# Kernel optimization log

Hardware: AMD Instinct MI355X
Metric: run time of the kernel (lower is better)

The kernel has to match this reference:

```python
import jax, jax.numpy as jnp
import numpy as np

N = 131072
HIDDEN = 20
N_HID = 7  # layers [3, 20*8, 2] -> 9 Linear layers: in(3,20), 7 hidden(20,20), out(20,2)


def _xavier(k, fan_in, fan_out):
    lim = np.sqrt(6.0 / (fan_in + fan_out)).astype(np.float32)
    return jax.random.uniform(k, (fan_in, fan_out), jnp.float32, -lim, lim)


def setup_inputs() -> dict:
    key = jax.random.key(0)
    ks = jax.random.split(key, 6 + N_HID)
    x = jax.random.normal(ks[0], (N, 1), jnp.float32)
    y = jax.random.normal(ks[1], (N, 1), jnp.float32)
    t = jax.random.normal(ks[2], (N, 1), jnp.float32)
    W_in = _xavier(ks[3], 3, HIDDEN)
    b_in = jnp.zeros((HIDDEN,), jnp.float32)
    W_hid = jnp.stack([_xavier(ks[4 + i], HIDDEN, HIDDEN) for i in range(N_HID)])
    b_hid = jnp.zeros((N_HID, HIDDEN), jnp.float32)
    W_out = _xavier(ks[4 + N_HID], HIDDEN, 2)
    b_out = jnp.zeros((2,), jnp.float32)
    lam1 = jnp.array([1.0], jnp.float32)   # lambda_1 (convective coefficient)
    lam2 = jnp.array([0.01], jnp.float32)  # lambda_2 (viscosity)
    return {"x": x, "y": y, "t": t, "W_in": W_in, "b_in": b_in,
            "W_hid": W_hid, "b_hid": b_hid, "W_out": W_out, "b_out": b_out,
            "lam1": lam1, "lam2": lam2}


def reference(x, y, t, W_in, b_in, W_hid, b_hid, W_out, b_out, lam1, lam2):
    z = jnp.concatenate([x, y, t], axis=1)  # (N, 3)

    def net(zz):  # zz: (3,) -> (2,) = (psi, p)
        h = jnp.tanh(zz @ W_in + b_in)
        for i in range(N_HID):
            h = jnp.tanh(h @ W_hid[i] + b_hid[i])
        return h @ W_out + b_out

    psi_fn = lambda zz: net(zz)[0]
    p_fn = lambda zz: net(zz)[1]
    g_psi = jax.grad(psi_fn)          # (3,): psi_x, psi_y, psi_t
    H_psi = jax.jacfwd(g_psi)         # (3,3): H[a,b] = psi_{ab}
    T_psi = jax.jacfwd(H_psi)         # (3,3,3): T[a,b,c] = psi_{abc}
    g_p = jax.grad(p_fn)              # (3,): p_x, p_y, p_t

    def per_point(zz):
        pv = p_fn(zz)
        gp = g_p(zz)
        g = g_psi(zz)
        H = H_psi(zz)
        T = T_psi(zz)
        # u = psi_y, v = -psi_x (axis 0=x, 1=y, 2=t)
        return jnp.stack([
            g[1], -g[0], pv,                # u, v, p
            H[1, 2], H[1, 0], H[1, 1],      # u_t, u_x, u_y
            T[1, 0, 0], T[1, 1, 1],         # u_xx, u_yy
            -H[0, 2], -H[0, 0], -H[0, 1],   # v_t, v_x, v_y
            -T[0, 0, 0], -T[0, 1, 1],       # v_xx, v_yy
            gp[0], gp[1],                   # p_x, p_y
        ])

    D = jax.vmap(per_point)(z)  # (N, 15)
    (u, v, p, u_t, u_x, u_y, u_xx, u_yy,
     v_t, v_x, v_y, v_xx, v_yy, p_x, p_y) = [D[:, i:i + 1] for i in range(15)]
    l1 = lam1[0]
    l2 = lam2[0]
    f_u = u_t + l1 * (u * u_x + v * u_y) + p_x - l2 * (u_xx + u_yy)
    f_v = v_t + l1 * (u * v_x + v * v_y) + p_y - l2 * (v_xx + v_yy)
    return (u, v, p, f_u, f_v)
```

## Files before the change

### kernel.cpp

```cpp
#include <hip/hip_runtime.h>

typedef float  f32x4  __attribute__((ext_vector_type(4)));
typedef short  bf16x8 __attribute__((ext_vector_type(8)));
typedef unsigned int u32;
typedef u32 u32x4 __attribute__((ext_vector_type(4)));

#define HID  20
#define NLAY 7
#define NC   11
#define PTS  16

__device__ __forceinline__ float tanh_derivs(float a, float& d1, float& d2, float& d3) {
    const float e = __expf(2.0f * a);
    const float s = 1.0f - __fdividef(2.0f, e + 1.0f);
    d1 = 1.0f - s * s;
    d2 = -2.0f * s * d1;
    d3 = -2.0f * (d1 * d1 + s * d2);
    return s;
}

__device__ __forceinline__ void jet_activate(const float* a, float* nv) {
    float d1, d2, d3;
    const float s = tanh_derivs(a[0], d1, d2, d3);
    const float gx = a[1], gy = a[2], gt = a[3];
    const float hxx = a[4], hxy = a[5], hyy = a[6];
    const float hxt = a[7], hyt = a[8];
    const float g2 = gx * gx + gy * gy;
    nv[0] = s;
    nv[1] = d1 * gx;  nv[2] = d1 * gy;  nv[3] = d1 * gt;
    nv[4] = fmaf(d2, gx * gx, d1 * hxx);
    nv[5] = fmaf(d2, gx * gy, d1 * hxy);
    nv[6] = fmaf(d2, gy * gy, d1 * hyy);
    nv[7] = fmaf(d2, gx * gt, d1 * hxt);
    nv[8] = fmaf(d2, gy * gt, d1 * hyt);
    nv[9]  = d3 * gx * g2 + d2 * (3.f * gx * hxx + 2.f * gy * hxy + gx * hyy) + d1 * a[9];
    nv[10] = d3 * gy * g2 + d2 * (3.f * gy * hyy + 2.f * gx * hxy + gy * hxx) + d1 * a[10];
}

__device__ __forceinline__ void pack_pair(float v0, float v1, u32& wh, u32& wl) {
    const u32 b0 = __float_as_uint(v0);
    const u32 b1 = __float_as_uint(v1);
    wh = (b0 >> 16) | (b1 & 0xFFFF0000u);
    const float l0 = v0 - __uint_as_float(b0 & 0xFFFF0000u);
    const float l1 = v1 - __uint_as_float(b1 & 0xFFFF0000u);
    wl = (__float_as_uint(l0) >> 16) | (__float_as_uint(l1) & 0xFFFF0000u);
}

__device__ __forceinline__ void input_neuron(int j, float xv, float yv, float tv,
                                             const float* __restrict__ W_in,
                                             const float* __restrict__ b_in, float* nv) {
    const float w0 = W_in[j], w1 = W_in[HID + j], w2 = W_in[2 * HID + j];
    const float a0 = fmaf(xv, w0, fmaf(yv, w1, fmaf(tv, w2, b_in[j])));
    float d1, d2, d3;
    const float s = tanh_derivs(a0, d1, d2, d3);
    const float g2w = w0 * w0 + w1 * w1;
    nv[0] = s;        nv[1] = d1 * w0;  nv[2] = d1 * w1;  nv[3] = d1 * w2;
    nv[4] = d2 * w0 * w0; nv[5] = d2 * w0 * w1; nv[6] = d2 * w1 * w1;
    nv[7] = d2 * w0 * w2; nv[8] = d2 * w1 * w2;
    nv[9] = d3 * w0 * g2w; nv[10] = d3 * w1 * g2w;
}

__global__ void wfrag_setup(const float* __restrict__ W_hid,
                            const float* __restrict__ b_hid,
                            unsigned* __restrict__ wsu)
{
    const int l = threadIdx.x;
    const int g = l >> 4, m = l & 15;
    for (int layer = 0; layer < NLAY; ++layer) {
        for (int jt = 0; jt < 2; ++jt) {
            const int j = jt * 16 + m;
            unsigned hi[8], lo[8];
            for (int e = 0; e < 8; ++e) {
                const int k = (e < 4) ? (4 * g + e) : (16 + 4 * g + (e - 4));
                float w = 0.0f;
                if (j < HID) {
                    if (k < HID)       w = W_hid[(layer * HID + k) * HID + j];
                    else if (k == HID) w = b_hid[layer * HID + j];
                }
                const unsigned hb = __float_as_uint(w) & 0xFFFF0000u;
                const float lf = w - __uint_as_float(hb);
                hi[e] = hb >> 16;
                lo[e] = __float_as_uint(lf) >> 16;
            }
            unsigned* ph = wsu + (((layer * 2 + jt) * 2 + 0) * 64 + l) * 4;
            unsigned* pl = wsu + (((layer * 2 + jt) * 2 + 1) * 64 + l) * 4;
            for (int r = 0; r < 4; ++r) {
                ph[r] = hi[2 * r] | (hi[2 * r + 1] << 16);
                pl[r] = lo[2 * r] | (lo[2 * r + 1] << 16);
            }
        }
    }
}

__global__ void __launch_bounds__(64)
pinn_mfma_reg(const float* __restrict__ xs, const float* __restrict__ ys, const float* __restrict__ ts,
              const float* __restrict__ W_in, const float* __restrict__ b_in,
              const float* __restrict__ W_out, const float* __restrict__ b_out,
              const float* __restrict__ lam1p, const float* __restrict__ lam2p,
              const unsigned* __restrict__ wsu,
              float* __restrict__ out, int N)
{
    const int l  = threadIdx.x;
    const int g  = l >> 4, pt = l & 15;
    const int idx0 = blockIdx.x * PTS;
    const int pi = min(idx0 + pt, N - 1);

    u32x4 Bh[NC], Bl[NC];

    const float xv = xs[pi], yv = ys[pi], tv = ts[pi];
    #pragma unroll
    for (int pr = 0; pr < 2; ++pr) {
        float nvA[NC], nvB[NC];
        input_neuron(4 * g + 2 * pr,     xv, yv, tv, W_in, b_in, nvA);
        input_neuron(4 * g + 2 * pr + 1, xv, yv, tv, W_in, b_in, nvB);
        #pragma unroll
        for (int c = 0; c < NC; ++c) {
            u32 th, tl;
            pack_pair(nvA[c], nvB[c], th, tl);
            Bh[c][pr] = th; Bl[c][pr] = tl;
        }
    }
    if (g == 0) {
        #pragma unroll
        for (int pr = 0; pr < 2; ++pr) {
            float nvA[NC], nvB[NC];
            input_neuron(16 + 2 * pr,     xv, yv, tv, W_in, b_in, nvA);
            input_neuron(16 + 2 * pr + 1, xv, yv, tv, W_in, b_in, nvB);
            #pragma unroll
            for (int c = 0; c < NC; ++c) {
                u32 th, tl;
                pack_pair(nvA[c], nvB[c], th, tl);
                Bh[c][2 + pr] = th; Bl[c][2 + pr] = tl;
            }
        }
    } else {
        #pragma unroll
        for (int c = 0; c < NC; ++c) { Bh[c][2] = 0u; Bh[c][3] = 0u; Bl[c][2] = 0u; Bl[c][3] = 0u; }
    }
    Bh[0][2] = (g == 1) ? 0x3F80u : Bh[0][2];
    Bl[0][2] = (g == 1) ? 0u      : Bl[0][2];

    const u32x4* wp = (const u32x4*)wsu;
    u32x4 f0 = wp[((0 * 2 + 0) * 2 + 0) * 64 + l];
    u32x4 f1 = wp[((0 * 2 + 0) * 2 + 1) * 64 + l];
    u32x4 f2 = wp[((0 * 2 + 1) * 2 + 0) * 64 + l];
    u32x4 f3 = wp[((0 * 2 + 1) * 2 + 1) * 64 + l];

    #pragma unroll 1
    for (int layer = 0; layer < NLAY; ++layer) {
        const int nl = (layer + 1 < NLAY) ? layer + 1 : layer;
        u32x4 n0 = wp[((nl * 2 + 0) * 2 + 0) * 64 + l];
        u32x4 n1 = wp[((nl * 2 + 0) * 2 + 1) * 64 + l];
        u32x4 n2 = wp[((nl * 2 + 1) * 2 + 0) * 64 + l];
        u32x4 n3 = wp[((nl * 2 + 1) * 2 + 1) * 64 + l];

        const bf16x8 ah0 = __builtin_bit_cast(bf16x8, f0);
        const bf16x8 al0 = __builtin_bit_cast(bf16x8, f1);
        const bf16x8 ah1 = __builtin_bit_cast(bf16x8, f2);
        const bf16x8 al1 = __builtin_bit_cast(bf16x8, f3);

        f32x4 acc1[NC], acc2[NC];
        #pragma unroll
        for (int c = 0; c < NC; ++c) {
            const bf16x8 bh = __builtin_bit_cast(bf16x8, Bh[c]);
            const bf16x8 bl = __builtin_bit_cast(bf16x8, Bl[c]);
            const f32x4 z = (f32x4){0.f, 0.f, 0.f, 0.f};
            f32x4 a1 = __builtin_amdgcn_mfma_f32_16x16x32_bf16(ah0, bh, z, 0, 0, 0);
            a1 = __builtin_amdgcn_mfma_f32_16x16x32_bf16(ah0, bl, a1, 0, 0, 0);
            a1 = __builtin_amdgcn_mfma_f32_16x16x32_bf16(al0, bh, a1, 0, 0, 0);
            acc1[c] = a1;
            f32x4 a2 = __builtin_amdgcn_mfma_f32_16x16x32_bf16(ah1, bh, z, 0, 0, 0);
            a2 = __builtin_amdgcn_mfma_f32_16x16x32_bf16(ah1, bl, a2, 0, 0, 0);
            a2 = __builtin_amdgcn_mfma_f32_16x16x32_bf16(al1, bh, a2, 0, 0, 0);
            acc2[c] = a2;
        }

        #pragma unroll
        for (int pr = 0; pr < 2; ++pr) {
            float aA[NC], aB[NC], nvA[NC], nvB[NC];
            #pragma unroll
            for (int c = 0; c < NC; ++c) { aA[c] = acc1[c][2 * pr]; aB[c] = acc1[c][2 * pr + 1]; }
            jet_activate(aA, nvA);
            jet_activate(aB, nvB);
            #pragma unroll
            for (int c = 0; c < NC; ++c) {
                u32 th, tl;
                pack_pair(nvA[c], nvB[c], th, tl);
                Bh[c][pr] = th; Bl[c][pr] = tl;
            }
        }
        #pragma unroll
        for (int pr = 0; pr < 2; ++pr) {
            float aA[NC], aB[NC], nvA[NC], nvB[NC];
            #pragma unroll
            for (int c = 0; c < NC; ++c) { aA[c] = acc2[c][2 * pr]; aB[c] = acc2[c][2 * pr + 1]; }
            jet_activate(aA, nvA);
            jet_activate(aB, nvB);
            #pragma unroll
            for (int c = 0; c < NC; ++c) {
                u32 th, tl;
                pack_pair(nvA[c], nvB[c], th, tl);
                Bh[c][2 + pr] = th; Bl[c][2 + pr] = tl;
            }
        }
        Bh[0][2] = (g == 1) ? 0x3F80u : Bh[0][2];
        Bl[0][2] = (g == 1) ? 0u      : Bl[0][2];

        f0 = n0; f1 = n1; f2 = n2; f3 = n3;
    }

    float su = 0, sv = 0, sp = 0, spx = 0, spy = 0, svx = 0;
    float sux = 0, suy = 0, svt = 0, sut = 0, slx = 0, sly = 0;

    #pragma unroll
    for (int q = 0; q < 4; ++q) {
        {
            const int j = 4 * g + q;
            const float w0 = W_out[2 * j], w1 = W_out[2 * j + 1];
            float r[NC];
            #pragma unroll
            for (int c = 0; c < NC; ++c) {
                if (c == 3) { r[c] = 0.0f; continue; }
                const u32 wh = Bh[c][q >> 1], wl = Bl[c][q >> 1];
                const u32 hh = (q & 1) ? (wh & 0xFFFF0000u) : (wh << 16);
                const u32 ll = (q & 1) ? (wl & 0xFFFF0000u) : (wl << 16);
                r[c] = __uint_as_float(hh) + __uint_as_float(ll);
            }
            sp  = fmaf(w1, r[0], sp);
            sv  = fmaf(w0, r[1], sv);    spx = fmaf(w1, r[1], spx);
            su  = fmaf(w0, r[2], su);    spy = fmaf(w1, r[2], spy);
            svx = fmaf(w0, r[4], svx);
            sux = fmaf(w0, r[5], sux);
            suy = fmaf(w0, r[6], suy);
            svt = fmaf(w0, r[7], svt);
            sut = fmaf(w0, r[8], sut);
            slx = fmaf(w0, r[9], slx);
            sly = fmaf(w0, r[10], sly);
        }
        {
            const int j2 = 16 + 4 * g + q;
            const int jc = (j2 < HID) ? j2 : 0;
            const float valid = (j2 < HID) ? 1.0f : 0.0f;
            const float w0 = W_out[2 * jc] * valid, w1 = W_out[2 * jc + 1] * valid;
            float r[NC];
            #pragma unroll
            for (int c = 0; c < NC; ++c) {
                if (c == 3) { r[c] = 0.0f; continue; }
                const u32 wh = Bh[c][2 + (q >> 1)], wl = Bl[c][2 + (q >> 1)];
                const u32 hh = (q & 1) ? (wh & 0xFFFF0000u) : (wh << 16);
                const u32 ll = (q & 1) ? (wl & 0xFFFF0000u) : (wl << 16);
                r[c] = __uint_as_float(hh) + __uint_as_float(ll);
            }
            sp  = fmaf(w1, r[0], sp);
            sv  = fmaf(w0, r[1], sv);    spx = fmaf(w1, r[1], spx);
            su  = fmaf(w0, r[2], su);    spy = fmaf(w1, r[2], spy);
            svx = fmaf(w0, r[4], svx);
            sux = fmaf(w0, r[5], sux);
            suy = fmaf(w0, r[6], suy);
            svt = fmaf(w0, r[7], svt);
            sut = fmaf(w0, r[8], sut);
            slx = fmaf(w0, r[9], slx);
            sly = fmaf(w0, r[10], sly);
        }
    }

    #define RED_(x) x += __shfl_xor(x, 16); x += __shfl_xor(x, 32)
    RED_(su); RED_(sv); RED_(sp); RED_(spx); RED_(spy); RED_(svx);
    RED_(sux); RED_(suy); RED_(svt); RED_(sut); RED_(slx); RED_(sly);
    #undef RED_

    if (g == 0 && idx0 + pt < N) {
        const float l1 = lam1p[0], l2 = lam2p[0];
        const float u = su, v = -sv, p = sp + b_out[1];
        const float fu = sut + l1 * (u * sux + v * suy) + spx - l2 * sly;
        const float fv = -svt + l1 * (u * (-svx) + v * (-sux)) + spy + l2 * slx;
        out[idx0 + pt]         = u;
        out[N + idx0 + pt]     = v;
        out[2 * N + idx0 + pt] = p;
        out[3 * N + idx0 + pt] = fu;
        out[4 * N + idx0 + pt] = fv;
    }
}

extern "C" void kernel_launch(void* const* d_in, const int* in_sizes, int n_in,
                              void* d_out, int out_size, void* d_ws, size_t ws_size,
                              hipStream_t stream) {
    const float* xs    = (const float*)d_in[0];
    const float* ys    = (const float*)d_in[1];
    const float* ts    = (const float*)d_in[2];
    const float* W_in  = (const float*)d_in[3];
    const float* b_in  = (const float*)d_in[4];
    const float* W_hid = (const float*)d_in[5];
    const float* b_hid = (const float*)d_in[6];
    const float* W_out = (const float*)d_in[7];
    const float* b_out = (const float*)d_in[8];
    const float* lam1  = (const float*)d_in[9];
    const float* lam2  = (const float*)d_in[10];
    float* out = (float*)d_out;

    const int N = in_sizes[0];
    wfrag_setup<<<1, 64, 0, stream>>>(W_hid, b_hid, (unsigned*)d_ws);
    const int grid = (N + PTS - 1) / PTS;
    pinn_mfma_reg<<<grid, 64, 0, stream>>>(xs, ys, ts, W_in, b_in, W_out, b_out,
                                           lam1, lam2, (const unsigned*)d_ws, out, N);
}
```

Before: 136.4 us.

## Drop low-bf16 split for third-derivative channels and peel final layer

Packing now uses the hardware v_cvt_pk_bf16_f32 instruction instead of manual bit masking. The two third-derivative channels (9,10) are kept only as a single bf16 high part, which removes their low-part MFMAs and packing work in every layer. The last hidden layer is peeled out of the loop and its activations are fed straight into the output projection in fp32, skipping the final pack and unpack. The risk is reduced precision in the third-derivative terms, which feed the viscosity part of the residual.

```diff
diff --git a/kernel.cpp b/kernel.cpp
--- a/kernel.cpp
+++ b/kernel.cpp
@@ -37,13 +37,17 @@
     nv[10] = d3 * gy * g2 + d2 * (3.f * gy * hyy + 2.f * gx * hxy + gy * hxx) + d1 * a[10];
 }
 
+__device__ __forceinline__ u32 cvt_pk_bf16(float a, float b) {
+    u32 r;
+    asm("v_cvt_pk_bf16_f32 %0, %1, %2" : "=v"(r) : "v"(a), "v"(b));
+    return r;
+}
+
 __device__ __forceinline__ void pack_pair(float v0, float v1, u32& wh, u32& wl) {
-    const u32 b0 = __float_as_uint(v0);
-    const u32 b1 = __float_as_uint(v1);
-    wh = (b0 >> 16) | (b1 & 0xFFFF0000u);
-    const float l0 = v0 - __uint_as_float(b0 & 0xFFFF0000u);
-    const float l1 = v1 - __uint_as_float(b1 & 0xFFFF0000u);
-    wl = (__float_as_uint(l0) >> 16) | (__float_as_uint(l1) & 0xFFFF0000u);
+    wh = cvt_pk_bf16(v0, v1);
+    const float h0 = __uint_as_float(wh << 16);
+    const float h1 = __uint_as_float(wh & 0xFFFF0000u);
+    wl = cvt_pk_bf16(v0 - h0, v1 - h1);
 }
 
 __device__ __forceinline__ void input_neuron(int j, float xv, float yv, float tv,
@@ -115,9 +119,13 @@
         input_neuron(4 * g + 2 * pr + 1, xv, yv, tv, W_in, b_in, nvB);
         #pragma unroll
         for (int c = 0; c < NC; ++c) {
-            u32 th, tl;
-            pack_pair(nvA[c], nvB[c], th, tl);
-            Bh[c][pr] = th; Bl[c][pr] = tl;
+            if (c < 9) {
+                u32 th, tl;
+                pack_pair(nvA[c], nvB[c], th, tl);
+                Bh[c][pr] = th; Bl[c][pr] = tl;
+            } else {
+                Bh[c][pr] = cvt_pk_bf16(nvA[c], nvB[c]);
+            }
         }
     }
     if (g == 0) {
@@ -128,9 +136,13 @@
             input_neuron(16 + 2 * pr + 1, xv, yv, tv, W_in, b_in, nvB);
             #pragma unroll
             for (int c = 0; c < NC; ++c) {
-                u32 th, tl;
-                pack_pair(nvA[c], nvB[c], th, tl);
-                Bh[c][2 + pr] = th; Bl[c][2 + pr] = tl;
+                if (c < 9) {
+                    u32 th, tl;
+                    pack_pair(nvA[c], nvB[c], th, tl);
+                    Bh[c][2 + pr] = th; Bl[c][2 + pr] = tl;
+                } else {
+                    Bh[c][2 + pr] = cvt_pk_bf16(nvA[c], nvB[c]);
+                }
             }
         }
     } else {
@@ -141,18 +153,18 @@
     Bl[0][2] = (g == 1) ? 0u      : Bl[0][2];
 
     const u32x4* wp = (const u32x4*)wsu;
-    u32x4 f0 = wp[((0 * 2 + 0) * 2 + 0) * 64 + l];
-    u32x4 f1 = wp[((0 * 2 + 0) * 2 + 1) * 64 + l];
-    u32x4 f2 = wp[((0 * 2 + 1) * 2 + 0) * 64 + l];
-    u32x4 f3 = wp[((0 * 2 + 1) * 2 + 1) * 64 + l];
+    u32x4 f0 = wp[0 * 64 + l];
+    u32x4 f1 = wp[1 * 64 + l];
+    u32x4 f2 = wp[2 * 64 + l];
+    u32x4 f3 = wp[3 * 64 + l];
 
     #pragma unroll 1
-    for (int layer = 0; layer < NLAY; ++layer) {
-        const int nl = (layer + 1 < NLAY) ? layer + 1 : layer;
-        u32x4 n0 = wp[((nl * 2 + 0) * 2 + 0) * 64 + l];
-        u32x4 n1 = wp[((nl * 2 + 0) * 2 + 1) * 64 + l];
-        u32x4 n2 = wp[((nl * 2 + 1) * 2 + 0) * 64 + l];
-        u32x4 n3 = wp[((nl * 2 + 1) * 2 + 1) * 64 + l];
+    for (int layer = 0; layer < NLAY - 1; ++layer) {
+        const int nl = layer + 1;
+        u32x4 n0 = wp[(nl * 4 + 0) * 64 + l];
+        u32x4 n1 = wp[(nl * 4 + 1) * 64 + l];
+        u32x4 n2 = wp[(nl * 4 + 2) * 64 + l];
+        u32x4 n3 = wp[(nl * 4 + 3) * 64 + l];
 
         const bf16x8 ah0 = __builtin_bit_cast(bf16x8, f0);
         const bf16x8 al0 = __builtin_bit_cast(bf16x8, f1);
@@ -163,15 +175,17 @@
         #pragma unroll
         for (int c = 0; c < NC; ++c) {
             const bf16x8 bh = __builtin_bit_cast(bf16x8, Bh[c]);
-            const bf16x8 bl = __builtin_bit_cast(bf16x8, Bl[c]);
             const f32x4 z = (f32x4){0.f, 0.f, 0.f, 0.f};
             f32x4 a1 = __builtin_amdgcn_mfma_f32_16x16x32_bf16(ah0, bh, z, 0, 0, 0);
-            a1 = __builtin_amdgcn_mfma_f32_16x16x32_bf16(ah0, bl, a1, 0, 0, 0);
+            f32x4 a2 = __builtin_amdgcn_mfma_f32_16x16x32_bf16(ah1, bh, z, 0, 0, 0);
+            if (c < 9) {
+                const bf16x8 bl = __builtin_bit_cast(bf16x8, Bl[c]);
+                a1 = __builtin_amdgcn_mfma_f32_16x16x32_bf16(ah0, bl, a1, 0, 0, 0);
+                a2 = __builtin_amdgcn_mfma_f32_16x16x32_bf16(ah1, bl, a2, 0, 0, 0);
+            }
             a1 = __builtin_amdgcn_mfma_f32_16x16x32_bf16(al0, bh, a1, 0, 0, 0);
+            a2 = __builtin_amdgcn_mfma_f32_16x16x32_bf16(al1, bh, a2, 0, 0, 0);
             acc1[c] = a1;
-            f32x4 a2 = __builtin_amdgcn_mfma_f32_16x16x32_bf16(ah1, bh, z, 0, 0, 0);
-            a2 = __builtin_amdgcn_mfma_f32_16x16x32_bf16(ah1, bl, a2, 0, 0, 0);
-            a2 = __builtin_amdgcn_mfma_f32_16x16x32_bf16(al1, bh, a2, 0, 0, 0);
             acc2[c] = a2;
         }
 
@@ -184,9 +198,13 @@
             jet_activate(aB, nvB);
             #pragma unroll
             for (int c = 0; c < NC; ++c) {
-                u32 th, tl;
-                pack_pair(nvA[c], nvB[c], th, tl);
-                Bh[c][pr] = th; Bl[c][pr] = tl;
+                if (c < 9) {
+                    u32 th, tl;
+                    pack_pair(nvA[c], nvB[c], th, tl);
+                    Bh[c][pr] = th; Bl[c][pr] = tl;
+                } else {
+                    Bh[c][pr] = cvt_pk_bf16(nvA[c], nvB[c]);
+                }
             }
         }
         #pragma unroll
@@ -198,9 +216,13 @@
             jet_activate(aB, nvB);
             #pragma unroll
             for (int c = 0; c < NC; ++c) {
-                u32 th, tl;
-                pack_pair(nvA[c], nvB[c], th, tl);
-                Bh[c][2 + pr] = th; Bl[c][2 + pr] = tl;
+                if (c < 9) {
+                    u32 th, tl;
+                    pack_pair(nvA[c], nvB[c], th, tl);
+                    Bh[c][2 + pr] = th; Bl[c][2 + pr] = tl;
+                } else {
+                    Bh[c][2 + pr] = cvt_pk_bf16(nvA[c], nvB[c]);
+                }
             }
         }
         Bh[0][2] = (g == 1) ? 0x3F80u : Bh[0][2];
@@ -211,56 +233,69 @@
 
     float su = 0, sv = 0, sp = 0, spx = 0, spy = 0, svx = 0;
     float sux = 0, suy = 0, svt = 0, sut = 0, slx = 0, sly = 0;
-
-    #pragma unroll
-    for (int q = 0; q < 4; ++q) {
-        {
-            const int j = 4 * g + q;
+    {
+        const bf16x8 ah0 = __builtin_bit_cast(bf16x8, f0);
+        const bf16x8 al0 = __builtin_bit_cast(bf16x8, f1);
+        const bf16x8 ah1 = __builtin_bit_cast(bf16x8, f2);
+        const bf16x8 al1 = __builtin_bit_cast(bf16x8, f3);
+
+        f32x4 acc1[NC], acc2[NC];
+        #pragma unroll
+        for (int c = 0; c < NC; ++c) {
+            const bf16x8 bh = __builtin_bit_cast(bf16x8, Bh[c]);
+            const f32x4 z = (f32x4){0.f, 0.f, 0.f, 0.f};
+            f32x4 a1 = __builtin_amdgcn_mfma_f32_16x16x32_bf16(ah0, bh, z, 0, 0, 0);
+            f32x4 a2 = __builtin_amdgcn_mfma_f32_16x16x32_bf16(ah1, bh, z, 0, 0, 0);
+            if (c < 9) {
+                const bf16x8 bl = __builtin_bit_cast(bf16x8, Bl[c]);
+                a1 = __builtin_amdgcn_mfma_f32_16x16x32_bf16(ah0, bl, a1, 0, 0, 0);
+                a2 = __builtin_amdgcn_mfma_f32_16x16x32_bf16(ah1, bl, a2, 0, 0, 0);
+            }
+            a1 = __builtin_amdgcn_mfma_f32_16x16x32_bf16(al0, bh, a1, 0, 0, 0);
+            a2 = __builtin_amdgcn_mfma_f32_16x16x32_bf16(al1, bh, a2, 0, 0, 0);
+            acc1[c] = a1;
+            acc2[c] = a2;
+        }
+
+        #pragma unroll
+        for (int s = 0; s < 4; ++s) {
+            float a[NC], nv[NC];
+            #pragma unroll
+            for (int c = 0; c < NC; ++c) a[c] = acc1[c][s];
+            jet_activate(a, nv);
+            const int j = 4 * g + s;
             const float w0 = W_out[2 * j], w1 = W_out[2 * j + 1];
-            float r[NC];
-            #pragma unroll
-            for (int c = 0; c < NC; ++c) {
-                if (c == 3) { r[c] = 0.0f; continue; }
-                const u32 wh = Bh[c][q >> 1], wl = Bl[c][q >> 1];
-                const u32 hh = (q & 1) ? (wh & 0xFFFF0000u) : (wh << 16);
-                const u32 ll = (q & 1) ? (wl & 0xFFFF0000u) : (wl << 16);
-                r[c] = __uint_as_float(hh) + __uint_as_float(ll);
-            }
-            sp  = fmaf(w1, r[0], sp);
-            sv  = fmaf(w0, r[1], sv);    spx = fmaf(w1, r[1], spx);
-            su  = fmaf(w0, r[2], su);    spy = fmaf(w1, r[2], spy);
-            svx = fmaf(w0, r[4], svx);
-            sux = fmaf(w0, r[5], sux);
-            suy = fmaf(w0, r[6], suy);
-            svt = fmaf(w0, r[7], svt);
-            sut = fmaf(w0, r[8], sut);
-            slx = fmaf(w0, r[9], slx);
-            sly = fmaf(w0, r[10], sly);
-        }
-        {
-            const int j2 = 16 + 4 * g + q;
+            sp  = fmaf(w1, nv[0], sp);
+            sv  = fmaf(w0, nv[1], sv);    spx = fmaf(w1, nv[1], spx);
+            su  = fmaf(w0, nv[2], su);    spy = fmaf(w1, nv[2], spy);
+            svx = fmaf(w0, nv[4], svx);
+            sux = fmaf(w0, nv[5], sux);
+            suy = fmaf(w0, nv[6], suy);
+            svt = fmaf(w0, nv[7], svt);
+            sut = fmaf(w0, nv[8], sut);
+            slx = fmaf(w0, nv[9], slx);
+            sly = fmaf(w0, nv[10], sly);
+        }
+        #pragma unroll
+        for (int s = 0; s < 4; ++s) {
+            float a[NC], nv[NC];
+            #pragma unroll
+            for (int c = 0; c < NC; ++c) a[c] = acc2[c][s];
+            jet_activate(a, nv);
+            const int j2 = 16 + 4 * g + s;
             const int jc = (j2 < HID) ? j2 : 0;
             const float valid = (j2 < HID) ? 1.0f : 0.0f;
             const float w0 = W_out[2 * jc] * valid, w1 = W_out[2 * jc + 1] * valid;
-            float r[NC];
-            #pragma unroll
-            for (int c = 0; c < NC; ++c) {
-                if (c == 3) { r[c] = 0.0f; continue; }
-                const u32 wh = Bh[c][2 + (q >> 1)], wl = Bl[c][2 + (q >> 1)];
-                const u32 hh = (q & 1) ? (wh & 0xFFFF0000u) : (wh << 16);
-                const u32 ll = (q & 1) ? (wl & 0xFFFF0000u) : (wl << 16);
-                r[c] = __uint_as_float(hh) + __uint_as_float(ll);
-            }
-            sp  = fmaf(w1, r[0], sp);
-            sv  = fmaf(w0, r[1], sv);    spx = fmaf(w1, r[1], spx);
-            su  = fmaf(w0, r[2], su);    spy = fmaf(w1, r[2], spy);
-            svx = fmaf(w0, r[4], svx);
-            sux = fmaf(w0, r[5], sux);
-            suy = fmaf(w0, r[6], suy);
-            svt = fmaf(w0, r[7], svt);
-            sut = fmaf(w0, r[8], sut);
-            slx = fmaf(w0, r[9], slx);
-            sly = fmaf(w0, r[10], sly);
+            sp  = fmaf(w1, nv[0], sp);
+            sv  = fmaf(w0, nv[1], sv);    spx = fmaf(w1, nv[1], spx);
+            su  = fmaf(w0, nv[2], su);    spy = fmaf(w1, nv[2], spy);
+            svx = fmaf(w0, nv[4], svx);
+            sux = fmaf(w0, nv[5], sux);
+            suy = fmaf(w0, nv[6], suy);
+            svt = fmaf(w0, nv[7], svt);
+            sut = fmaf(w0, nv[8], sut);
+            slx = fmaf(w0, nv[9], slx);
+            sly = fmaf(w0, nv[10], sly);
         }
     }
 
```

Measured after the change: 125.0 us. -8.4%, faster.
